# Kernel optimization log

Hardware: AMD Instinct MI355X
Metric: run time of the kernel (lower is better)

## Reference

```python
import jax, jax.numpy as jnp
import numpy as np

B, S, UNITS = 32, 2048, 512
D = 2 * UNITS  # 1024


def setup_inputs() -> dict:
    key = jax.random.key(0)
    ks = jax.random.split(key, 12)
    s = 1.0 / np.sqrt(D)
    mask = (jax.random.uniform(ks[0], (B, S)) < 0.9).astype(jnp.float32)
    mask = mask.at[:, 0].set(1.0)  # guarantee no all-zero row
    return {
        "dec_hidden": jax.random.normal(ks[1], (2, B, UNITS), dtype=jnp.float32),
        "enc_output": jax.random.normal(ks[2], (B, S, D), dtype=jnp.float32),
        "enc_pad_mask": mask,
        "prev_coverage": jax.random.uniform(ks[3], (B, S), dtype=jnp.float32) * 0.1,
        "Wh": jax.random.uniform(ks[4], (D, D), minval=-s, maxval=s),
        "bh": jax.random.uniform(ks[5], (D,), minval=-s, maxval=s),
        "Ws": jax.random.uniform(ks[6], (D, D), minval=-s, maxval=s),
        "bs": jax.random.uniform(ks[7], (D,), minval=-s, maxval=s),
        "Wc": jax.random.uniform(ks[8], (D, 1), minval=-1.0, maxval=1.0),
        "bc": jax.random.uniform(ks[9], (D,), minval=-1.0, maxval=1.0),
        "v": jax.random.uniform(ks[10], (1, D), minval=-s, maxval=s),
        "bv": jax.random.uniform(ks[11], (1,), minval=-s, maxval=s),
        "use_coverage": 1,
    }


def reference(dec_hidden, enc_output, enc_pad_mask, prev_coverage,
              Wh, bh, Ws, bs, Wc, bc, v, bv, use_coverage):
    # dec_hidden: (2, B, units) -> (B, 1, 2*units)
    dec = jnp.transpose(dec_hidden, (1, 0, 2)).reshape(dec_hidden.shape[1], 1, -1)
    enc_features = jnp.einsum('bsd,ed->bse', enc_output, Wh) + bh  # (B,S,D)
    dec_features = jnp.einsum('bod,ed->boe', dec, Ws) + bs          # (B,1,D)
    att_inputs = enc_features + dec_features
    if use_coverage:
        # Linear(1 -> D) applied to prev_coverage[..., None]
        coverage_features = prev_coverage[:, :, None] * Wc[:, 0][None, None, :] + bc
        att_inputs = att_inputs + coverage_features
    score = jnp.einsum('bsd,od->bso', jnp.tanh(att_inputs), v) + bv  # (B,S,1)
    attention_weights = jax.nn.softmax(score, axis=1)[..., 0]        # (B,S)
    attention_weights = attention_weights * enc_pad_mask
    attention_weights = attention_weights / jnp.sum(attention_weights, axis=1, keepdims=True)
    context_vector = jnp.einsum('bs,bsd->bd', attention_weights, enc_output)
    if use_coverage:
        coverage_vector = prev_coverage + attention_weights
        return context_vector, attention_weights, coverage_vector
    return context_vector, attention_weights
```

## Files before the change

kernel.cpp:

```cpp
#include <hip/hip_runtime.h>
#include <hip/hip_bf16.h>

#define BATCH 32
#define SEQ   2048
#define DIM   1024

typedef __attribute__((ext_vector_type(4))) float f32x4;
typedef __attribute__((ext_vector_type(8))) short short8;

static __device__ __forceinline__ ushort f2bf(float x) {
    __hip_bfloat16 h = __float2bfloat16(x);
    union { __hip_bfloat16 h; ushort u; } cv; cv.h = h;
    return cv.u;
}

static __device__ __forceinline__ void gll16(const void* g, void* l) {
    __builtin_amdgcn_global_load_lds(
        (const __attribute__((address_space(1))) void*)g,
        (__attribute__((address_space(3))) void*)l, 16, 0, 0);
}

__global__ __launch_bounds__(256) void kWhPack(const float* __restrict__ Wh,
                                               ushort* __restrict__ whbp) {
    int g = blockIdx.x * 256 + threadIdx.x;
    int l  = g & 63;
    int kb = (g >> 6) & 31;
    int eb = g >> 11;
    int e  = eb * 16 + (l & 15);
    int k0 = kb * 32 + (l >> 4) * 8;
    const float* src = Wh + (size_t)e * DIM + k0;
    float4 a = *(const float4*)src;
    float4 b = *(const float4*)(src + 4);
    union { ushort us[8]; uint4 u4; } pk;
    pk.us[0] = f2bf(a.x); pk.us[1] = f2bf(a.y); pk.us[2] = f2bf(a.z); pk.us[3] = f2bf(a.w);
    pk.us[4] = f2bf(b.x); pk.us[5] = f2bf(b.y); pk.us[6] = f2bf(b.z); pk.us[7] = f2bf(b.w);
    *(uint4*)(whbp + (size_t)g * 8) = pk.u4;
}

__global__ __launch_bounds__(256) void kBase(const float* __restrict__ dh,
                                             const float* __restrict__ Ws,
                                             const float* __restrict__ bs,
                                             const float* __restrict__ bh,
                                             const float* __restrict__ bc,
                                             const int* __restrict__ uc,
                                             float* __restrict__ base) {
    __shared__ float dec[8][DIM];
    int ec = blockIdx.x >> 2;
    int bg = blockIdx.x & 3;
    int b0 = bg * 8, e0 = ec * 32;
    int tid = threadIdx.x;
    for (int i = tid; i < 8 * DIM; i += 256) {
        int bb = i >> 10, d = i & 1023;
        float vdec = (d < 512) ? dh[(b0 + bb) * 512 + d]
                               : dh[BATCH * 512 + (b0 + bb) * 512 + d - 512];
        dec[bb][d] = vdec;
    }
    __syncthreads();
    int el = tid >> 3, ds = tid & 7;
    int e = e0 + el;
    float acc[8] = {0.f, 0.f, 0.f, 0.f, 0.f, 0.f, 0.f, 0.f};
    const float* wrow = Ws + (size_t)e * DIM;
    for (int i = 0; i < 128; ++i) {
        int d = i * 8 + ds;
        float wv = wrow[d];
#pragma unroll
        for (int bb = 0; bb < 8; ++bb) acc[bb] += wv * dec[bb][d];
    }
#pragma unroll
    for (int bb = 0; bb < 8; ++bb) {
        float s = acc[bb];
        s += __shfl_xor(s, 1); s += __shfl_xor(s, 2); s += __shfl_xor(s, 4);
        acc[bb] = s;
    }
    if (ds == 0) {
        float bias = bs[e] + bh[e] + ((*uc) ? bc[e] : 0.0f);
#pragma unroll
        for (int bb = 0; bb < 8; ++bb) base[(b0 + bb) * DIM + e] = acc[bb] + bias;
    }
}

__global__ __launch_bounds__(512, 2) void kScore(const float* __restrict__ enc,
                                                 const ushort* __restrict__ whbp,
                                                 const float* __restrict__ base,
                                                 const float* __restrict__ pc,
                                                 const float* __restrict__ Wc,
                                                 const float* __restrict__ vv,
                                                 const int* __restrict__ uc,
                                                 float* __restrict__ scorep) {
    __shared__ ushort Al[2][16384];
    __shared__ ushort Bl[2][16384];
    __shared__ float pcl[256];
    __shared__ float red[4][256];

    const int tid = threadIdx.x;
    const int w = tid >> 6, lane = tid & 63;
    const int q = lane >> 4, l15 = lane & 15;
    const int wm = w >> 2, wn = w & 3;

    const int x = blockIdx.x & 7;
    const int j = blockIdx.x >> 3;
    const int ms = x * 32 + (j >> 2);
    const int nb = j & 3;
    const int b = ms >> 3;
    const int s0 = (ms & 7) << 8;

    const float* Ab = enc + ((size_t)(b * SEQ + s0)) * DIM;
    if (tid < 256) pcl[tid] = pc[b * SEQ + s0 + tid];

    const float* agp[4];
    int adst[4];
#pragma unroll
    for (int i = 0; i < 4; ++i) {
        int fA = i * 8 + w, mt = fA >> 1, kb = fA & 1;
        int row = mt * 16 + l15, kk = kb * 32 + q * 8;
        agp[i] = Ab + (size_t)row * DIM + kk;
        adst[i] = fA * 512 + lane * 8;
    }
    const ushort* bsrc[4];
    int bdst[4];
#pragma unroll
    for (int c = 0; c < 4; ++c) {
        int fB = c * 8 + w, ebl = fB >> 1, kbit = fB & 1;
        bsrc[c] = whbp + ((size_t)((nb * 16 + ebl) * 32 + kbit)) * 512 + lane * 8;
        bdst[c] = fB * 512;
    }

    f32x4 acc[8][4] = {};
    float4 rA[8];

#define CVT_WRITE(BUF) do { \
    _Pragma("unroll") \
    for (int i = 0; i < 4; ++i) { \
        union { ushort us[8]; uint4 u4; } pk_; \
        float4 lo = rA[2*i], hi = rA[2*i+1]; \
        pk_.us[0]=f2bf(lo.x); pk_.us[1]=f2bf(lo.y); pk_.us[2]=f2bf(lo.z); pk_.us[3]=f2bf(lo.w); \
        pk_.us[4]=f2bf(hi.x); pk_.us[5]=f2bf(hi.y); pk_.us[6]=f2bf(hi.z); pk_.us[7]=f2bf(hi.w); \
        *(uint4*)&Al[BUF][adst[i]] = pk_.u4; \
    } } while (0)

#define ALOAD(KT) do { \
    _Pragma("unroll") \
    for (int i = 0; i < 4; ++i) { \
        const float* p_ = agp[i] + (KT) * 64; \
        rA[2*i] = *(const float4*)p_; rA[2*i+1] = *(const float4*)(p_ + 4); \
    } } while (0)

#define GLLB(KT, BUF) do { \
    _Pragma("unroll") \
    for (int c = 0; c < 4; ++c) \
        gll16(bsrc[c] + (size_t)(KT) * 1024, &Bl[BUF][bdst[c]]); \
    } while (0)

#define MFMA_PHASE(BUF, KB) do { \
    short8 a_[8], b_[4]; \
    _Pragma("unroll") \
    for (int mf = 0; mf < 8; ++mf) \
        a_[mf] = *(const short8*)&Al[BUF][(((wm<<3)+mf)*2+(KB))*512 + (lane<<3)]; \
    _Pragma("unroll") \
    for (int ef = 0; ef < 4; ++ef) \
        b_[ef] = *(const short8*)&Bl[BUF][(((wn<<2)+ef)*2+(KB))*512 + (lane<<3)]; \
    __builtin_amdgcn_s_setprio(1); \
    _Pragma("unroll") \
    for (int ef = 0; ef < 4; ++ef) \
        _Pragma("unroll") \
        for (int mf = 0; mf < 8; ++mf) \
            acc[mf][ef] = __builtin_amdgcn_mfma_f32_16x16x32_bf16(a_[mf], b_[ef], acc[mf][ef], 0, 0, 0); \
    __builtin_amdgcn_s_setprio(0); \
    } while (0)

    ALOAD(0);
    GLLB(0, 0);
    CVT_WRITE(0);
    ALOAD(1);
    __syncthreads();
    GLLB(1, 1);

    for (int kt = 0; kt < 16; ++kt) {
        const int cur = kt & 1, nxt = cur ^ 1;
        MFMA_PHASE(cur, 0);
        if (kt < 15) {
            CVT_WRITE(nxt);
            if (kt < 14) ALOAD(kt + 2);
        }
        MFMA_PHASE(cur, 1);
        if (kt < 15) {
            asm volatile("s_waitcnt lgkmcnt(0)" ::: "memory");
            if (kt < 14) { asm volatile("s_waitcnt vmcnt(8)" ::: "memory"); }
            else         { asm volatile("s_waitcnt vmcnt(0)" ::: "memory"); }
            __builtin_amdgcn_sched_barrier(0);
            __builtin_amdgcn_s_barrier();
            __builtin_amdgcn_sched_barrier(0);
            if (kt < 14) GLLB(kt + 2, cur);
        }
    }

    const float ucf = (float)(*uc);
    float basee[4], ve[4], wce[4];
#pragma unroll
    for (int ef = 0; ef < 4; ++ef) {
        int e = (nb << 8) + ((wn << 2) + ef) * 16 + l15;
        basee[ef] = base[b * DIM + e];
        ve[ef] = vv[e];
        wce[ef] = Wc[e] * ucf;
    }
#pragma unroll
    for (int mf = 0; mf < 8; ++mf) {
#pragma unroll
        for (int r = 0; r < 4; ++r) {
            int rl = (wm << 7) + (mf << 4) + (q << 2) + r;
            float p = pcl[rl];
            float sp = 0.f;
#pragma unroll
            for (int ef = 0; ef < 4; ++ef) {
                float xv = acc[mf][ef][r] + basee[ef] + p * wce[ef];
                float t = 1.0f - 2.0f / (1.0f + __expf(2.0f * xv));
                sp += t * ve[ef];
            }
            sp += __shfl_xor(sp, 1);
            sp += __shfl_xor(sp, 2);
            sp += __shfl_xor(sp, 4);
            sp += __shfl_xor(sp, 8);
            if (l15 == 0) red[wn][rl] = sp;
        }
    }
    __syncthreads();
    if (tid < 256) {
        float s = (red[0][tid] + red[1][tid]) + (red[2][tid] + red[3][tid]);
        scorep[nb * (BATCH * SEQ) + b * SEQ + s0 + tid] = s;
    }
}

__global__ __launch_bounds__(512) void kSoftmax(const float* __restrict__ scorep,
                                                const float* __restrict__ mask,
                                                const float* __restrict__ pc,
                                                float* __restrict__ att,
                                                float* __restrict__ cov,
                                                int write_cov) {
    __shared__ float rmax[8], rsum[8];
    const int BS = BATCH * SEQ;
    int b = blockIdx.x, tid = threadIdx.x;
    int wv = tid >> 6, ln = tid & 63;
    float x[4];
#pragma unroll
    for (int i = 0; i < 4; ++i) {
        int idx = b * SEQ + tid + i * 512;
        x[i] = (scorep[idx] + scorep[BS + idx]) + (scorep[2 * BS + idx] + scorep[3 * BS + idx]);
    }
    float m = fmaxf(fmaxf(x[0], x[1]), fmaxf(x[2], x[3]));
#pragma unroll
    for (int o = 1; o < 64; o <<= 1) m = fmaxf(m, __shfl_xor(m, o));
    if (ln == 0) rmax[wv] = m;
    __syncthreads();
    m = rmax[0];
#pragma unroll
    for (int i = 1; i < 8; ++i) m = fmaxf(m, rmax[i]);

    float ms[4], wm[4];
#pragma unroll
    for (int i = 0; i < 4; ++i) ms[i] = mask[b * SEQ + tid + i * 512];
    float s = 0.f;
#pragma unroll
    for (int i = 0; i < 4; ++i) { wm[i] = __expf(x[i] - m) * ms[i]; s += wm[i]; }
#pragma unroll
    for (int o = 1; o < 64; o <<= 1) s += __shfl_xor(s, o);
    if (ln == 0) rsum[wv] = s;
    __syncthreads();
    s = 0.f;
#pragma unroll
    for (int i = 0; i < 8; ++i) s += rsum[i];
    float inv = 1.0f / s;
#pragma unroll
    for (int i = 0; i < 4; ++i) {
        float wf = wm[i] * inv;
        att[b * SEQ + tid + i * 512] = wf;
        if (write_cov) cov[b * SEQ + tid + i * 512] = pc[b * SEQ + tid + i * 512] + wf;
    }
}

__global__ __launch_bounds__(256) void kCtxPart(const float* __restrict__ enc,
                                                const float* __restrict__ att,
                                                float* __restrict__ part) {
    __shared__ float wl[64];
    int bx = blockIdx.x;
    int b = bx >> 5, sc = bx & 31;
    int tid = threadIdx.x;
    if (tid < 64) wl[tid] = att[b * SEQ + sc * 64 + tid];
    __syncthreads();
    const float* basep = enc + ((size_t)(b * SEQ + sc * 64)) * DIM + tid * 4;
    float4 acc = {0.f, 0.f, 0.f, 0.f};
#pragma unroll 4
    for (int i = 0; i < 64; ++i) {
        float w = wl[i];
        float4 xv = *(const float4*)(basep + (size_t)i * DIM);
        acc.x += w * xv.x; acc.y += w * xv.y; acc.z += w * xv.z; acc.w += w * xv.w;
    }
    *(float4*)(part + (size_t)bx * DIM + tid * 4) = acc;
}

__global__ __launch_bounds__(256) void kCtxReduce(const float* __restrict__ part,
                                                  float* __restrict__ ctx) {
    int g = blockIdx.x * 256 + threadIdx.x;
    int b = g >> 10, d = g & 1023;
    float s = 0.f;
#pragma unroll
    for (int i = 0; i < 32; ++i) s += part[((size_t)(b * 32 + i) << 10) + d];
    ctx[g] = s;
}

extern "C" void kernel_launch(void* const* d_in, const int* in_sizes, int n_in,
                              void* d_out, int out_size, void* d_ws, size_t ws_size,
                              hipStream_t stream) {
    const float* dh   = (const float*)d_in[0];
    const float* enc  = (const float*)d_in[1];
    const float* mask = (const float*)d_in[2];
    const float* pc   = (const float*)d_in[3];
    const float* Wh   = (const float*)d_in[4];
    const float* bh   = (const float*)d_in[5];
    const float* Ws   = (const float*)d_in[6];
    const float* bs   = (const float*)d_in[7];
    const float* Wc   = (const float*)d_in[8];
    const float* bc   = (const float*)d_in[9];
    const float* vv   = (const float*)d_in[10];
    const int* uc     = (const int*)d_in[12];

    float* ctx = (float*)d_out;
    float* att = ctx + BATCH * DIM;
    float* cov = att + BATCH * SEQ;
    int write_cov = (out_size >= BATCH * (DIM + 2 * SEQ)) ? 1 : 0;

    ushort* whbp  = (ushort*)d_ws;
    float* base   = (float*)((char*)d_ws + 2u * 1024u * 1024u);
    float* scorep = base + BATCH * DIM;
    float* part   = scorep + 4 * BATCH * SEQ;

    kWhPack<<<512, 256, 0, stream>>>(Wh, whbp);
    kBase<<<128, 256, 0, stream>>>(dh, Ws, bs, bh, bc, uc, base);
    kScore<<<1024, 512, 0, stream>>>(enc, whbp, base, pc, Wc, vv, uc, scorep);
    kSoftmax<<<BATCH, 512, 0, stream>>>(scorep, mask, pc, att, cov, write_cov);
    kCtxPart<<<1024, 256, 0, stream>>>(enc, att, part);
    kCtxReduce<<<128, 256, 0, stream>>>(part, ctx);
}
```

Baseline: 289.9 us.

## Pre-pack encoder output to bf16 tiles and shrink score GEMM tiles

Adds a separate kernel that converts the full fp32 encoder output into a bf16 MFMA-fragment layout in workspace. The score GEMM then loads both operands with direct global-to-LDS copies instead of converting A in registers. The GEMM tile is halved (128x128, 256 threads, 4096 blocks), so softmax now sums eight partial score slices. This removes in-loop conversion and register staging, at the cost of an extra full pass that reads 256MB of encoder data and writes 128MB of packed bf16.

```diff
diff --git a/kernel.cpp b/kernel.cpp
--- a/kernel.cpp
+++ b/kernel.cpp
@@ -20,21 +20,42 @@
         (__attribute__((address_space(3))) void*)l, 16, 0, 0);
 }
 
+__global__ __launch_bounds__(256) void kAPack(const float* __restrict__ enc,
+                                              ushort* __restrict__ apk) {
+    int g = blockIdx.x * 256 + threadIdx.x;
+    int lane = g & 63;
+    int frag = (g >> 6) & 31;
+    int kt   = (g >> 11) & 15;
+    int strip = g >> 15;
+    int mt = frag >> 1, kb = frag & 1;
+    int row = (strip << 8) + (mt << 4) + (lane & 15);
+    int k0  = (kt << 6) + (kb << 5) + ((lane >> 4) << 3);
+    const float* src = enc + (size_t)row * DIM + k0;
+    float4 a = *(const float4*)src;
+    float4 b = *(const float4*)(src + 4);
+    union { ushort us[8]; uint4 u4; } pk;
+    pk.us[0] = f2bf(a.x); pk.us[1] = f2bf(a.y); pk.us[2] = f2bf(a.z); pk.us[3] = f2bf(a.w);
+    pk.us[4] = f2bf(b.x); pk.us[5] = f2bf(b.y); pk.us[6] = f2bf(b.z); pk.us[7] = f2bf(b.w);
+    *(uint4*)(apk + (size_t)g * 8) = pk.u4;
+}
+
 __global__ __launch_bounds__(256) void kWhPack(const float* __restrict__ Wh,
-                                               ushort* __restrict__ whbp) {
+                                               ushort* __restrict__ bpk) {
     int g = blockIdx.x * 256 + threadIdx.x;
-    int l  = g & 63;
-    int kb = (g >> 6) & 31;
-    int eb = g >> 11;
-    int e  = eb * 16 + (l & 15);
-    int k0 = kb * 32 + (l >> 4) * 8;
+    int lane = g & 63;
+    int frag = (g >> 6) & 31;
+    int kt   = (g >> 11) & 15;
+    int nb   = g >> 15;
+    int ebl = frag >> 1, kbit = frag & 1;
+    int e  = (nb << 8) + (ebl << 4) + (lane & 15);
+    int k0 = (kt << 6) + (kbit << 5) + ((lane >> 4) << 3);
     const float* src = Wh + (size_t)e * DIM + k0;
     float4 a = *(const float4*)src;
     float4 b = *(const float4*)(src + 4);
     union { ushort us[8]; uint4 u4; } pk;
     pk.us[0] = f2bf(a.x); pk.us[1] = f2bf(a.y); pk.us[2] = f2bf(a.z); pk.us[3] = f2bf(a.w);
     pk.us[4] = f2bf(b.x); pk.us[5] = f2bf(b.y); pk.us[6] = f2bf(b.z); pk.us[7] = f2bf(b.w);
-    *(uint4*)(whbp + (size_t)g * 8) = pk.u4;
+    *(uint4*)(bpk + (size_t)g * 8) = pk.u4;
 }
 
 __global__ __launch_bounds__(256) void kBase(const float* __restrict__ dh,
@@ -79,118 +100,88 @@
     }
 }
 
-__global__ __launch_bounds__(512, 2) void kScore(const float* __restrict__ enc,
-                                                 const ushort* __restrict__ whbp,
+__global__ __launch_bounds__(256, 2) void kScore(const ushort* __restrict__ apk,
+                                                 const ushort* __restrict__ bpk,
                                                  const float* __restrict__ base,
                                                  const float* __restrict__ pc,
                                                  const float* __restrict__ Wc,
                                                  const float* __restrict__ vv,
                                                  const int* __restrict__ uc,
                                                  float* __restrict__ scorep) {
-    __shared__ ushort Al[2][16384];
-    __shared__ ushort Bl[2][16384];
-    __shared__ float pcl[256];
-    __shared__ float red[4][256];
+    __shared__ ushort Al[2][8192];
+    __shared__ ushort Bl[2][8192];
+    __shared__ float red[2][128];
 
     const int tid = threadIdx.x;
     const int w = tid >> 6, lane = tid & 63;
     const int q = lane >> 4, l15 = lane & 15;
-    const int wm = w >> 2, wn = w & 3;
+    const int wm = w >> 1, wn = w & 1;
 
     const int x = blockIdx.x & 7;
-    const int j = blockIdx.x >> 3;
-    const int ms = x * 32 + (j >> 2);
-    const int nb = j & 3;
-    const int b = ms >> 3;
-    const int s0 = (ms & 7) << 8;
-
-    const float* Ab = enc + ((size_t)(b * SEQ + s0)) * DIM;
-    if (tid < 256) pcl[tid] = pc[b * SEQ + s0 + tid];
-
-    const float* agp[4];
-    int adst[4];
-#pragma unroll
-    for (int i = 0; i < 4; ++i) {
-        int fA = i * 8 + w, mt = fA >> 1, kb = fA & 1;
-        int row = mt * 16 + l15, kk = kb * 32 + q * 8;
-        agp[i] = Ab + (size_t)row * DIM + kk;
-        adst[i] = fA * 512 + lane * 8;
-    }
-    const ushort* bsrc[4];
-    int bdst[4];
-#pragma unroll
-    for (int c = 0; c < 4; ++c) {
-        int fB = c * 8 + w, ebl = fB >> 1, kbit = fB & 1;
-        bsrc[c] = whbp + ((size_t)((nb * 16 + ebl) * 32 + kbit)) * 512 + lane * 8;
-        bdst[c] = fB * 512;
-    }
-
-    f32x4 acc[8][4] = {};
-    float4 rA[8];
-
-#define CVT_WRITE(BUF) do { \
+    const int jj = blockIdx.x >> 3;
+    const int ms = (x << 6) + (jj >> 3);
+    const int nbk = jj & 7;
+    const int b = ms >> 4;
+    const int s0 = (ms & 15) << 7;
+
+    const ushort* abase = apk + ((size_t)(ms >> 1) << 18) + ((size_t)(ms & 1) << 13);
+    const ushort* bbase = bpk + ((size_t)(nbk >> 1) << 18) + ((size_t)(nbk & 1) << 13);
+
+#define STAGE(KT, BUF) do { \
+    const ushort* as_ = abase + ((size_t)(KT) << 14); \
+    const ushort* bs_ = bbase + ((size_t)(KT) << 14); \
     _Pragma("unroll") \
-    for (int i = 0; i < 4; ++i) { \
-        union { ushort us[8]; uint4 u4; } pk_; \
-        float4 lo = rA[2*i], hi = rA[2*i+1]; \
-        pk_.us[0]=f2bf(lo.x); pk_.us[1]=f2bf(lo.y); pk_.us[2]=f2bf(lo.z); pk_.us[3]=f2bf(lo.w); \
-        pk_.us[4]=f2bf(hi.x); pk_.us[5]=f2bf(hi.y); pk_.us[6]=f2bf(hi.z); pk_.us[7]=f2bf(hi.w); \
-        *(uint4*)&Al[BUF][adst[i]] = pk_.u4; \
+    for (int c_ = 0; c_ < 4; ++c_) { \
+        int f_ = (c_ << 2) + w; \
+        gll16(as_ + (f_ << 9) + (lane << 3), &Al[BUF][f_ << 9]); \
+        gll16(bs_ + (f_ << 9) + (lane << 3), &Bl[BUF][f_ << 9]); \
     } } while (0)
 
-#define ALOAD(KT) do { \
+    f32x4 acc[4][4] = {};
+
+#define MFMA_PHASE(BUF, KB) do { \
+    short8 a_[4], b_[4]; \
     _Pragma("unroll") \
-    for (int i = 0; i < 4; ++i) { \
-        const float* p_ = agp[i] + (KT) * 64; \
-        rA[2*i] = *(const float4*)p_; rA[2*i+1] = *(const float4*)(p_ + 4); \
-    } } while (0)
-
-#define GLLB(KT, BUF) do { \
-    _Pragma("unroll") \
-    for (int c = 0; c < 4; ++c) \
-        gll16(bsrc[c] + (size_t)(KT) * 1024, &Bl[BUF][bdst[c]]); \
-    } while (0)
-
-#define MFMA_PHASE(BUF, KB) do { \
-    short8 a_[8], b_[4]; \
-    _Pragma("unroll") \
-    for (int mf = 0; mf < 8; ++mf) \
-        a_[mf] = *(const short8*)&Al[BUF][(((wm<<3)+mf)*2+(KB))*512 + (lane<<3)]; \
+    for (int mf = 0; mf < 4; ++mf) \
+        a_[mf] = *(const short8*)&Al[BUF][(((((wm << 2) + mf) << 1) + (KB)) << 9) + (lane << 3)]; \
     _Pragma("unroll") \
     for (int ef = 0; ef < 4; ++ef) \
-        b_[ef] = *(const short8*)&Bl[BUF][(((wn<<2)+ef)*2+(KB))*512 + (lane<<3)]; \
+        b_[ef] = *(const short8*)&Bl[BUF][(((((wn << 2) + ef) << 1) + (KB)) << 9) + (lane << 3)]; \
     __builtin_amdgcn_s_setprio(1); \
     _Pragma("unroll") \
     for (int ef = 0; ef < 4; ++ef) \
         _Pragma("unroll") \
-        for (int mf = 0; mf < 8; ++mf) \
+        for (int mf = 0; mf < 4; ++mf) \
             acc[mf][ef] = __builtin_amdgcn_mfma_f32_16x16x32_bf16(a_[mf], b_[ef], acc[mf][ef], 0, 0, 0); \
     __builtin_amdgcn_s_setprio(0); \
     } while (0)
 
-    ALOAD(0);
-    GLLB(0, 0);
-    CVT_WRITE(0);
-    ALOAD(1);
-    __syncthreads();
-    GLLB(1, 1);
+    STAGE(0, 0);
+    STAGE(1, 1);
+    __builtin_amdgcn_sched_barrier(0);
+    asm volatile("s_waitcnt vmcnt(8)" ::: "memory");
+    __builtin_amdgcn_sched_barrier(0);
+    __builtin_amdgcn_s_barrier();
+    __builtin_amdgcn_sched_barrier(0);
 
     for (int kt = 0; kt < 16; ++kt) {
-        const int cur = kt & 1, nxt = cur ^ 1;
+        const int cur = kt & 1;
         MFMA_PHASE(cur, 0);
-        if (kt < 15) {
-            CVT_WRITE(nxt);
-            if (kt < 14) ALOAD(kt + 2);
-        }
         MFMA_PHASE(cur, 1);
         if (kt < 15) {
-            asm volatile("s_waitcnt lgkmcnt(0)" ::: "memory");
-            if (kt < 14) { asm volatile("s_waitcnt vmcnt(8)" ::: "memory"); }
-            else         { asm volatile("s_waitcnt vmcnt(0)" ::: "memory"); }
             __builtin_amdgcn_sched_barrier(0);
             __builtin_amdgcn_s_barrier();
             __builtin_amdgcn_sched_barrier(0);
-            if (kt < 14) GLLB(kt + 2, cur);
+            if (kt < 14) {
+                STAGE(kt + 2, cur);
+                __builtin_amdgcn_sched_barrier(0);
+                asm volatile("s_waitcnt vmcnt(8)" ::: "memory");
+            } else {
+                asm volatile("s_waitcnt vmcnt(0)" ::: "memory");
+            }
+            __builtin_amdgcn_sched_barrier(0);
+            __builtin_amdgcn_s_barrier();
+            __builtin_amdgcn_sched_barrier(0);
         }
     }
 
@@ -198,17 +189,17 @@
     float basee[4], ve[4], wce[4];
 #pragma unroll
     for (int ef = 0; ef < 4; ++ef) {
-        int e = (nb << 8) + ((wn << 2) + ef) * 16 + l15;
+        int e = (nbk << 7) + (wn << 6) + (ef << 4) + l15;
         basee[ef] = base[b * DIM + e];
         ve[ef] = vv[e];
         wce[ef] = Wc[e] * ucf;
     }
 #pragma unroll
-    for (int mf = 0; mf < 8; ++mf) {
+    for (int mf = 0; mf < 4; ++mf) {
 #pragma unroll
         for (int r = 0; r < 4; ++r) {
-            int rl = (wm << 7) + (mf << 4) + (q << 2) + r;
-            float p = pcl[rl];
+            int rl = (wm << 6) + (mf << 4) + (q << 2) + r;
+            float p = pc[b * SEQ + s0 + rl];
             float sp = 0.f;
 #pragma unroll
             for (int ef = 0; ef < 4; ++ef) {
@@ -224,10 +215,8 @@
         }
     }
     __syncthreads();
-    if (tid < 256) {
-        float s = (red[0][tid] + red[1][tid]) + (red[2][tid] + red[3][tid]);
-        scorep[nb * (BATCH * SEQ) + b * SEQ + s0 + tid] = s;
-    }
+    if (tid < 128)
+        scorep[nbk * (BATCH * SEQ) + b * SEQ + s0 + tid] = red[0][tid] + red[1][tid];
 }
 
 __global__ __launch_bounds__(512) void kSoftmax(const float* __restrict__ scorep,
@@ -244,7 +233,11 @@
 #pragma unroll
     for (int i = 0; i < 4; ++i) {
         int idx = b * SEQ + tid + i * 512;
-        x[i] = (scorep[idx] + scorep[BS + idx]) + (scorep[2 * BS + idx] + scorep[3 * BS + idx]);
+        float s01 = scorep[idx] + scorep[BS + idx];
+        float s23 = scorep[2 * BS + idx] + scorep[3 * BS + idx];
+        float s45 = scorep[4 * BS + idx] + scorep[5 * BS + idx];
+        float s67 = scorep[6 * BS + idx] + scorep[7 * BS + idx];
+        x[i] = (s01 + s23) + (s45 + s67);
     }
     float m = fmaxf(fmaxf(x[0], x[1]), fmaxf(x[2], x[3]));
 #pragma unroll
@@ -328,14 +321,16 @@
     float* cov = att + BATCH * SEQ;
     int write_cov = (out_size >= BATCH * (DIM + 2 * SEQ)) ? 1 : 0;
 
-    ushort* whbp  = (ushort*)d_ws;
-    float* base   = (float*)((char*)d_ws + 2u * 1024u * 1024u);
+    ushort* apk  = (ushort*)d_ws;
+    ushort* bpk  = apk + (size_t)BATCH * SEQ * DIM;
+    float* base   = (float*)(bpk + (size_t)DIM * DIM);
     float* scorep = base + BATCH * DIM;
-    float* part   = scorep + 4 * BATCH * SEQ;
-
-    kWhPack<<<512, 256, 0, stream>>>(Wh, whbp);
+    float* part   = scorep + 8 * BATCH * SEQ;
+
+    kAPack<<<32768, 256, 0, stream>>>(enc, apk);
+    kWhPack<<<512, 256, 0, stream>>>(Wh, bpk);
     kBase<<<128, 256, 0, stream>>>(dh, Ws, bs, bh, bc, uc, base);
-    kScore<<<1024, 512, 0, stream>>>(enc, whbp, base, pc, Wc, vv, uc, scorep);
+    kScore<<<4096, 256, 0, stream>>>(apk, bpk, base, pc, Wc, vv, uc, scorep);
     kSoftmax<<<BATCH, 512, 0, stream>>>(scorep, mask, pc, att, cov, write_cov);
     kCtxPart<<<1024, 256, 0, stream>>>(enc, att, part);
     kCtxReduce<<<128, 256, 0, stream>>>(part, ctx);
```

Measured after the change: 370.9 us. 1.28x slower.
